# Performance work log

Hardware: AMD Instinct MI355X
Metric: run time of the kernel (lower is better)

The kernel has to match this reference:

```python
import jax, jax.numpy as jnp
import numpy as np

B, I, O, DEG = 16384, 1024, 1024, 8

def setup_inputs() -> dict:
    key = jax.random.key(0)
    kx, kc = jax.random.split(key)
    x = jax.random.normal(kx, (B, I), dtype=jnp.float32)
    std = 1.0 / (I * (DEG + 1))
    cheby_coeffs = jax.random.normal(kc, (I, O, DEG + 1), dtype=jnp.float32) * std
    return {"x": x, "cheby_coeffs": cheby_coeffs}


def reference(x, cheby_coeffs):
    # Chebyshev basis: T_d(tanh(x)) = cos(d * acos(tanh(x)))
    deg = cheby_coeffs.shape[-1]
    arange = jnp.arange(deg, dtype=x.dtype)  # (D+1,)
    theta = jnp.arccos(jnp.tanh(x))          # (B, I)
    basis = jnp.cos(theta[:, :, None] * arange)  # (B, I, D+1)
    y = jnp.einsum('bid,iod->bo', basis, cheby_coeffs)
    return y
```

## Files before the change

kernel.cpp:

```cpp
#include <hip/hip_runtime.h>
#include <hip/hip_bf16.h>


#define WSCALE 4096.0f
#define INV_WSCALE (1.0f/4096.0f)

typedef _Float16 f16;
typedef __fp16   hf2  __attribute__((ext_vector_type(2)));
typedef _Float16 f16x8 __attribute__((ext_vector_type(8)));
typedef float    f32x4 __attribute__((ext_vector_type(4)));
typedef float    f32x16 __attribute__((ext_vector_type(16)));

union F16x8u { hf2 h2[4]; f16x8 v8; };

__global__ __launch_bounds__(256) void wt_transform(const float* __restrict__ cc,
                                                    f16* __restrict__ wt) {
  int t    = blockIdx.x * 256 + threadIdx.x;
  int j4   = t & 127;
  int grp  = t >> 7;
  int ncol = grp & 7;
  int rest = grp >> 3;
  int ic   = rest & 31;
  int d    = rest >> 5;
  int u    = j4 >> 5;
  int h    = (j4 >> 4) & 1;
  int r    = j4 & 15;
  int rk   = (r >> 1) & 3;
  size_t base = (size_t)(d * 32 + ic) * 32768 + (size_t)ncol * 4096 + (size_t)j4 * 32;
#pragma unroll
  for (int v = 0; v < 4; ++v) {
    int tt = v ^ rk;
    int q  = tt & 1, kl = tt >> 1;
    int o  = ncol * 128 + u * 32 + q * 16 + r;
    int ib = ic * 32 + h * 16 + kl * 8;
    f16x8 val;
#pragma unroll
    for (int e = 0; e < 8; ++e)
      val[e] = (f16)(cc[((size_t)(ib + e) * 1024 + o) * 9 + d] * WSCALE);
    *(f16x8*)(wt + base + v * 8) = val;
  }
}

__global__ __launch_bounds__(256) void t2_transform(const float* __restrict__ x,
                                                    f16* __restrict__ t2) {
  size_t gid = (size_t)blockIdx.x * 256 + threadIdx.x;
  const float* p = x + gid * 8;
  f32x4 a = *(const f32x4*)p;
  f32x4 b = *(const f32x4*)(p + 4);
  float tf[8];
#pragma unroll
  for (int e = 0; e < 8; ++e) {
    float xx = (e < 4) ? a[e] : b[e - 4];
    tf[e] = 1.f - 2.f * __builtin_amdgcn_rcpf(__expf(2.f * xx) + 1.f);
  }
  F16x8u u;
#pragma unroll
  for (int q = 0; q < 4; ++q)
    u.h2[q] = __builtin_amdgcn_cvt_pkrtz(tf[2 * q], tf[2 * q + 1]);
  f16x8 v = u.v8 + u.v8;
  *(f16x8*)(t2 + gid * 8) = v;
}

template <int PRET>
__global__ __launch_bounds__(512, 2) void cheby_gemm(const float* __restrict__ x,
                                                     const f16* __restrict__ t2g,
                                                     const f16* __restrict__ wt,
                                                     float* __restrict__ out) {
  __shared__ f16 bbuf[18][4096];

  const int tid  = threadIdx.x;
  const int wid  = tid >> 6;
  const int lane = tid & 63;
  const int lr   = lane & 31;
  const int lh   = lane >> 5;
  const int wm   = wid >> 1;
  const int wn   = wid & 1;
  const int mrow = blockIdx.x >> 3;
  const int ncol = blockIdx.x & 7;
  const int m0   = mrow * 256 + wm * 64;
  const int n0   = ncol * 128 + wn * 64;
  const int rbase = wn * 2048 + ((lane & 15) * 4 + ((lane >> 4) ^ ((lane >> 1) & 3))) * 8;

  auto stage = [&](int cn, int dn, int buf) {
    const f16* src = wt + (size_t)(dn * 32 + cn) * 32768 + (size_t)ncol * 4096;
    __builtin_amdgcn_global_load_lds(
        (const __attribute__((address_space(1))) unsigned*)(src + tid * 8),
        (__attribute__((address_space(3))) unsigned*)(&bbuf[buf][wid * 512]),
        16, 0, 0);
  };
  auto stage9 = [&](int cn, int b0) {
#pragma unroll
    for (int d = 0; d < 9; ++d) stage(cn, d, b0 + d);
  };

  f32x16 acc[2][2];
#pragma unroll
  for (int a = 0; a < 2; ++a)
#pragma unroll
    for (int b = 0; b < 2; ++b)
#pragma unroll
      for (int j = 0; j < 16; ++j) acc[a][b][j] = 0.f;

  const f16x8 ones  = {(f16)1,(f16)1,(f16)1,(f16)1,(f16)1,(f16)1,(f16)1,(f16)1};
  const f16x8 half8 = {(f16)0.5f,(f16)0.5f,(f16)0.5f,(f16)0.5f,
                       (f16)0.5f,(f16)0.5f,(f16)0.5f,(f16)0.5f};
  f16x8 t2v[2][2], t2n[2][2];
  f32x4 xf[2][2][2];

  auto loadx = [&](int cn) {
    if constexpr (PRET) {
#pragma unroll
      for (int mb = 0; mb < 2; ++mb)
#pragma unroll
        for (int h = 0; h < 2; ++h)
          t2n[mb][h] = *(const f16x8*)(t2g + (size_t)(m0 + mb * 32 + lr) * 1024
                                           + cn * 32 + h * 16 + lh * 8);
    } else {
#pragma unroll
      for (int mb = 0; mb < 2; ++mb)
#pragma unroll
        for (int h = 0; h < 2; ++h) {
          const float* p = x + (size_t)(m0 + mb * 32 + lr) * 1024 + cn * 32 + h * 16 + lh * 8;
          xf[mb][h][0] = *(const f32x4*)p;
          xf[mb][h][1] = *(const f32x4*)(p + 4);
        }
    }
  };
  auto dotanh = [&]() {
    if constexpr (!PRET) {
#pragma unroll
      for (int mb = 0; mb < 2; ++mb)
#pragma unroll
        for (int h = 0; h < 2; ++h) {
          float tf[8];
#pragma unroll
          for (int e = 0; e < 8; ++e) {
            float xx = (e < 4) ? xf[mb][h][0][e] : xf[mb][h][1][e - 4];
            tf[e] = 1.f - 2.f * __builtin_amdgcn_rcpf(__expf(2.f * xx) + 1.f);
          }
          F16x8u u;
#pragma unroll
          for (int q = 0; q < 4; ++q)
            u.h2[q] = __builtin_amdgcn_cvt_pkrtz(tf[2 * q], tf[2 * q + 1]);
          t2n[mb][h] = u.v8 + u.v8;
        }
    }
  };

#define REC(NEW, S1, S2)                                                       \
  _Pragma("unroll") for (int mb = 0; mb < 2; ++mb)                             \
    _Pragma("unroll") for (int h = 0; h < 2; ++h)                              \
      NEW[mb][h] = __builtin_elementwise_fma(t2v[mb][h], S1[mb][h], -S2[mb][h]);

#define CLUSTER(AF, DIDX)                                                      \
  {                                                                            \
    const f16* bb = &bbuf[0][0] + sbase + (DIDX) * 4096 + rbase;               \
    f16x8 bf[2][2];                                                            \
    _Pragma("unroll") for (int nb = 0; nb < 2; ++nb)                           \
      _Pragma("unroll") for (int h = 0; h < 2; ++h)                            \
        bf[nb][h] = *(const f16x8*)&bb[nb * 1024 + h * 512];                   \
    _Pragma("unroll") for (int nb = 0; nb < 2; ++nb)                           \
      _Pragma("unroll") for (int mb = 0; mb < 2; ++mb) {                       \
        acc[mb][nb] = __builtin_amdgcn_mfma_f32_32x32x16_f16(AF[mb][0], bf[nb][0], \
                                                             acc[mb][nb], 0, 0, 0); \
        acc[mb][nb] = __builtin_amdgcn_mfma_f32_32x32x16_f16(AF[mb][1], bf[nb][1], \
                                                             acc[mb][nb], 0, 0, 0); \
      }                                                                        \
  }

  stage9(0, 0);
  loadx(0);
  dotanh();

  f16x8 onesA[2][2];
#pragma unroll
  for (int mb = 0; mb < 2; ++mb)
#pragma unroll
    for (int h = 0; h < 2; ++h) onesA[mb][h] = ones;

  for (int c = 0; c < 32; ++c) {
    const bool lastc = (c == 31);
    const int  sbase = (c & 1) * 9 * 4096;
    const int  nbase = (1 - (c & 1)) * 9;

    if constexpr (PRET) asm volatile("s_waitcnt vmcnt(4)" ::: "memory");
    else                asm volatile("s_waitcnt vmcnt(8)" ::: "memory");
    __builtin_amdgcn_s_barrier();

    f16x8 A1[2][2], A2[2][2], A3[2][2], A4[2][2], A5[2][2], A6[2][2], A7[2][2], A8[2][2];
#pragma unroll
    for (int mb = 0; mb < 2; ++mb)
#pragma unroll
      for (int h = 0; h < 2; ++h) {
        t2v[mb][h] = t2n[mb][h];
        A1[mb][h]  = t2v[mb][h] * half8;
      }

    if (!lastc) {
      stage9(c + 1, nbase);
      loadx(c + 1);
    }

    CLUSTER(onesA, 0)
    CLUSTER(A1, 1)
    REC(A2, A1, onesA)  CLUSTER(A2, 2)
    REC(A3, A2, A1)     CLUSTER(A3, 3)
    REC(A4, A3, A2)     CLUSTER(A4, 4)
    REC(A5, A4, A3)     CLUSTER(A5, 5)
    REC(A6, A5, A4)     CLUSTER(A6, 6)
    REC(A7, A6, A5)     CLUSTER(A7, 7)
    REC(A8, A7, A6)     CLUSTER(A8, 8)

    if (!lastc) dotanh();
  }
#undef REC
#undef CLUSTER

#pragma unroll
  for (int mb = 0; mb < 2; ++mb)
#pragma unroll
    for (int nb = 0; nb < 2; ++nb)
#pragma unroll
      for (int j = 0; j < 16; ++j) {
        int row = m0 + mb * 32 + 4 * lh + (j & 3) + 8 * (j >> 2);
        int col = n0 + nb * 32 + lr;
        out[(size_t)row * 1024 + col] = acc[mb][nb][j] * INV_WSCALE;
      }
}

extern "C" void kernel_launch(void* const* d_in, const int* in_sizes, int n_in,
                              void* d_out, int out_size, void* d_ws, size_t ws_size,
                              hipStream_t stream) {
  const float* x  = (const float*)d_in[0];
  const float* cc = (const float*)d_in[1];
  f16*   wt  = (f16*)d_ws;
  f16*   t2  = (f16*)((char*)d_ws + 18874368);
  float* out = (float*)d_out;

  hipLaunchKernelGGL(wt_transform, dim3(1152), dim3(256), 0, stream, cc, wt);
  if (ws_size >= 52428800) {
    hipLaunchKernelGGL(t2_transform, dim3(8192), dim3(256), 0, stream, x, t2);
    hipLaunchKernelGGL((cheby_gemm<1>), dim3(512), dim3(512), 0, stream, x, t2, wt, out);
  } else {
    hipLaunchKernelGGL((cheby_gemm<0>), dim3(512), dim3(512), 0, stream, x, t2, wt, out);
  }
}
```

Before: 328.6 us.

## Software-pipeline LDS fragment loads and per-degree staging in pretransformed GEMM

The pretransformed-input GEMM path is split into its own kernel. It interleaves the per-degree global-to-LDS staging for the next chunk with the compute of the current chunk, waiting on individual degree buffers instead of all nine at once. B fragments are double-buffered in registers so LDS reads overlap the MFMAs, and MFMA blocks raise wave priority with s_setprio. The last chunk is peeled out of the loop. The finer barriers add sync overhead in exchange for better overlap of memory and compute.

```diff
diff --git a/kernel.cpp b/kernel.cpp
--- a/kernel.cpp
+++ b/kernel.cpp
@@ -61,9 +61,7 @@
   *(f16x8*)(t2 + gid * 8) = v;
 }
 
-template <int PRET>
-__global__ __launch_bounds__(512, 2) void cheby_gemm(const float* __restrict__ x,
-                                                     const f16* __restrict__ t2g,
+__global__ __launch_bounds__(512, 2) void cheby_gemm(const f16* __restrict__ t2g,
                                                      const f16* __restrict__ wt,
                                                      float* __restrict__ out) {
   __shared__ f16 bbuf[18][4096];
@@ -88,6 +86,165 @@
         (__attribute__((address_space(3))) unsigned*)(&bbuf[buf][wid * 512]),
         16, 0, 0);
   };
+
+  f32x16 acc[2][2];
+#pragma unroll
+  for (int a = 0; a < 2; ++a)
+#pragma unroll
+    for (int b = 0; b < 2; ++b)
+#pragma unroll
+      for (int j = 0; j < 16; ++j) acc[a][b][j] = 0.f;
+
+  const f16x8 ones  = {(f16)1,(f16)1,(f16)1,(f16)1,(f16)1,(f16)1,(f16)1,(f16)1};
+  const f16x8 half8 = {(f16)0.5f,(f16)0.5f,(f16)0.5f,(f16)0.5f,
+                       (f16)0.5f,(f16)0.5f,(f16)0.5f,(f16)0.5f};
+  f16x8 t2v[2][2], t2n[2][2];
+
+  auto loadx = [&](int cn) {
+#pragma unroll
+    for (int mb = 0; mb < 2; ++mb)
+#pragma unroll
+      for (int h = 0; h < 2; ++h)
+        t2n[mb][h] = *(const f16x8*)(t2g + (size_t)(m0 + mb * 32 + lr) * 1024
+                                         + cn * 32 + h * 16 + lh * 8);
+  };
+
+#define REC(NEW, S1, S2)                                                       \
+  _Pragma("unroll") for (int mb = 0; mb < 2; ++mb)                             \
+    _Pragma("unroll") for (int h = 0; h < 2; ++h)                              \
+      NEW[mb][h] = __builtin_elementwise_fma(t2v[mb][h], S1[mb][h], -S2[mb][h]);
+
+#define LOADB(BD, SB, DIDX)                                                    \
+  {                                                                            \
+    const f16* bb = &bbuf[0][0] + (SB) + (DIDX) * 4096 + rbase;                \
+    BD[0][0] = *(const f16x8*)&bb[0];    BD[0][1] = *(const f16x8*)&bb[512];   \
+    BD[1][0] = *(const f16x8*)&bb[1024]; BD[1][1] = *(const f16x8*)&bb[1536];  \
+  }
+
+#define MFMA8(AF, BD)                                                          \
+  {                                                                            \
+    __builtin_amdgcn_s_setprio(1);                                             \
+    _Pragma("unroll") for (int nb = 0; nb < 2; ++nb)                           \
+      _Pragma("unroll") for (int mb = 0; mb < 2; ++mb) {                       \
+        acc[mb][nb] = __builtin_amdgcn_mfma_f32_32x32x16_f16(AF[mb][0], BD[nb][0], \
+                                                             acc[mb][nb], 0, 0, 0); \
+        acc[mb][nb] = __builtin_amdgcn_mfma_f32_32x32x16_f16(AF[mb][1], BD[nb][1], \
+                                                             acc[mb][nb], 0, 0, 0); \
+      }                                                                        \
+    __builtin_amdgcn_s_setprio(0);                                             \
+  }
+
+#define VMB(N)                                                                 \
+  asm volatile("s_waitcnt vmcnt(" #N ")" ::: "memory");                        \
+  __builtin_amdgcn_s_barrier();
+
+#pragma unroll
+  for (int d = 0; d < 9; ++d) stage(0, d, d);
+  loadx(0);
+
+  f16x8 onesA[2][2];
+#pragma unroll
+  for (int mb = 0; mb < 2; ++mb)
+#pragma unroll
+    for (int h = 0; h < 2; ++h) onesA[mb][h] = ones;
+
+  f16x8 bfA[2][2], bfB[2][2];
+  f16x8 A1[2][2], A2[2][2], A3[2][2], A4[2][2], A5[2][2], A6[2][2], A7[2][2], A8[2][2];
+
+  for (int c = 0; c < 31; ++c) {
+    const int sbase = (c & 1) * 36864;
+    const int nbase = (1 - (c & 1)) * 9;
+
+    VMB(7)
+    LOADB(bfA, sbase, 0)
+#pragma unroll
+    for (int mb = 0; mb < 2; ++mb)
+#pragma unroll
+      for (int h = 0; h < 2; ++h) {
+        t2v[mb][h] = t2n[mb][h];
+        A1[mb][h]  = t2v[mb][h] * half8;
+      }
+    stage(c + 1, 0, nbase + 0);
+    loadx(c + 1);
+    LOADB(bfB, sbase, 1)
+    MFMA8(onesA, bfA)
+
+    VMB(11) stage(c + 1, 1, nbase + 1); LOADB(bfA, sbase, 2) REC(A2, A1, onesA) MFMA8(A1, bfB)
+    VMB(11) stage(c + 1, 2, nbase + 2); LOADB(bfB, sbase, 3) REC(A3, A2, A1)    MFMA8(A2, bfA)
+    VMB(11) stage(c + 1, 3, nbase + 3); LOADB(bfA, sbase, 4) REC(A4, A3, A2)    MFMA8(A3, bfB)
+    VMB(11) stage(c + 1, 4, nbase + 4); LOADB(bfB, sbase, 5) REC(A5, A4, A3)    MFMA8(A4, bfA)
+    VMB(11) stage(c + 1, 5, nbase + 5); LOADB(bfA, sbase, 6) REC(A6, A5, A4)    MFMA8(A5, bfB)
+    VMB(11) stage(c + 1, 6, nbase + 6); LOADB(bfB, sbase, 7) REC(A7, A6, A5)    MFMA8(A6, bfA)
+    VMB(11) stage(c + 1, 7, nbase + 7); LOADB(bfA, sbase, 8) REC(A8, A7, A6)    MFMA8(A7, bfB)
+
+    stage(c + 1, 8, nbase + 8);
+    MFMA8(A8, bfA)
+  }
+
+  {
+    const int sbase = 36864;
+    asm volatile("s_waitcnt vmcnt(0)" ::: "memory");
+    __builtin_amdgcn_s_barrier();
+    LOADB(bfA, sbase, 0)
+#pragma unroll
+    for (int mb = 0; mb < 2; ++mb)
+#pragma unroll
+      for (int h = 0; h < 2; ++h) {
+        t2v[mb][h] = t2n[mb][h];
+        A1[mb][h]  = t2v[mb][h] * half8;
+      }
+    LOADB(bfB, sbase, 1)
+    MFMA8(onesA, bfA)
+    LOADB(bfA, sbase, 2) REC(A2, A1, onesA) MFMA8(A1, bfB)
+    LOADB(bfB, sbase, 3) REC(A3, A2, A1)    MFMA8(A2, bfA)
+    LOADB(bfA, sbase, 4) REC(A4, A3, A2)    MFMA8(A3, bfB)
+    LOADB(bfB, sbase, 5) REC(A5, A4, A3)    MFMA8(A4, bfA)
+    LOADB(bfA, sbase, 6) REC(A6, A5, A4)    MFMA8(A5, bfB)
+    LOADB(bfB, sbase, 7) REC(A7, A6, A5)    MFMA8(A6, bfA)
+    LOADB(bfA, sbase, 8) REC(A8, A7, A6)    MFMA8(A7, bfB)
+    MFMA8(A8, bfA)
+  }
+#undef REC
+#undef LOADB
+#undef MFMA8
+#undef VMB
+
+#pragma unroll
+  for (int mb = 0; mb < 2; ++mb)
+#pragma unroll
+    for (int nb = 0; nb < 2; ++nb)
+#pragma unroll
+      for (int j = 0; j < 16; ++j) {
+        int row = m0 + mb * 32 + 4 * lh + (j & 3) + 8 * (j >> 2);
+        int col = n0 + nb * 32 + lr;
+        out[(size_t)row * 1024 + col] = acc[mb][nb][j] * INV_WSCALE;
+      }
+}
+
+__global__ __launch_bounds__(512, 2) void cheby_gemm_fb(const float* __restrict__ x,
+                                                        const f16* __restrict__ wt,
+                                                        float* __restrict__ out) {
+  __shared__ f16 bbuf[18][4096];
+  const int tid  = threadIdx.x;
+  const int wid  = tid >> 6;
+  const int lane = tid & 63;
+  const int lr   = lane & 31;
+  const int lh   = lane >> 5;
+  const int wm   = wid >> 1;
+  const int wn   = wid & 1;
+  const int mrow = blockIdx.x >> 3;
+  const int ncol = blockIdx.x & 7;
+  const int m0   = mrow * 256 + wm * 64;
+  const int n0   = ncol * 128 + wn * 64;
+  const int rbase = wn * 2048 + ((lane & 15) * 4 + ((lane >> 4) ^ ((lane >> 1) & 3))) * 8;
+
+  auto stage = [&](int cn, int dn, int buf) {
+    const f16* src = wt + (size_t)(dn * 32 + cn) * 32768 + (size_t)ncol * 4096;
+    __builtin_amdgcn_global_load_lds(
+        (const __attribute__((address_space(1))) unsigned*)(src + tid * 8),
+        (__attribute__((address_space(3))) unsigned*)(&bbuf[buf][wid * 512]),
+        16, 0, 0);
+  };
   auto stage9 = [&](int cn, int b0) {
 #pragma unroll
     for (int d = 0; d < 9; ++d) stage(cn, d, b0 + d);
@@ -108,50 +265,38 @@
   f32x4 xf[2][2][2];
 
   auto loadx = [&](int cn) {
-    if constexpr (PRET) {
-#pragma unroll
-      for (int mb = 0; mb < 2; ++mb)
-#pragma unroll
-        for (int h = 0; h < 2; ++h)
-          t2n[mb][h] = *(const f16x8*)(t2g + (size_t)(m0 + mb * 32 + lr) * 1024
-                                           + cn * 32 + h * 16 + lh * 8);
-    } else {
-#pragma unroll
-      for (int mb = 0; mb < 2; ++mb)
-#pragma unroll
-        for (int h = 0; h < 2; ++h) {
-          const float* p = x + (size_t)(m0 + mb * 32 + lr) * 1024 + cn * 32 + h * 16 + lh * 8;
-          xf[mb][h][0] = *(const f32x4*)p;
-          xf[mb][h][1] = *(const f32x4*)(p + 4);
+#pragma unroll
+    for (int mb = 0; mb < 2; ++mb)
+#pragma unroll
+      for (int h = 0; h < 2; ++h) {
+        const float* p = x + (size_t)(m0 + mb * 32 + lr) * 1024 + cn * 32 + h * 16 + lh * 8;
+        xf[mb][h][0] = *(const f32x4*)p;
+        xf[mb][h][1] = *(const f32x4*)(p + 4);
+      }
+  };
+  auto dotanh = [&]() {
+#pragma unroll
+    for (int mb = 0; mb < 2; ++mb)
+#pragma unroll
+      for (int h = 0; h < 2; ++h) {
+        float tf[8];
+#pragma unroll
+        for (int e = 0; e < 8; ++e) {
+          float xx = (e < 4) ? xf[mb][h][0][e] : xf[mb][h][1][e - 4];
+          tf[e] = 1.f - 2.f * __builtin_amdgcn_rcpf(__expf(2.f * xx) + 1.f);
         }
-    }
-  };
-  auto dotanh = [&]() {
-    if constexpr (!PRET) {
-#pragma unroll
-      for (int mb = 0; mb < 2; ++mb)
-#pragma unroll
-        for (int h = 0; h < 2; ++h) {
-          float tf[8];
-#pragma unroll
-          for (int e = 0; e < 8; ++e) {
-            float xx = (e < 4) ? xf[mb][h][0][e] : xf[mb][h][1][e - 4];
-            tf[e] = 1.f - 2.f * __builtin_amdgcn_rcpf(__expf(2.f * xx) + 1.f);
-          }
-          F16x8u u;
-#pragma unroll
-          for (int q = 0; q < 4; ++q)
-            u.h2[q] = __builtin_amdgcn_cvt_pkrtz(tf[2 * q], tf[2 * q + 1]);
-          t2n[mb][h] = u.v8 + u.v8;
-        }
-    }
+        F16x8u u;
+#pragma unroll
+        for (int q = 0; q < 4; ++q)
+          u.h2[q] = __builtin_amdgcn_cvt_pkrtz(tf[2 * q], tf[2 * q + 1]);
+        t2n[mb][h] = u.v8 + u.v8;
+      }
   };
 
 #define REC(NEW, S1, S2)                                                       \
   _Pragma("unroll") for (int mb = 0; mb < 2; ++mb)                             \
     _Pragma("unroll") for (int h = 0; h < 2; ++h)                              \
       NEW[mb][h] = __builtin_elementwise_fma(t2v[mb][h], S1[mb][h], -S2[mb][h]);
-
 #define CLUSTER(AF, DIDX)                                                      \
   {                                                                            \
     const f16* bb = &bbuf[0][0] + sbase + (DIDX) * 4096 + rbase;               \
@@ -180,11 +325,10 @@
 
   for (int c = 0; c < 32; ++c) {
     const bool lastc = (c == 31);
-    const int  sbase = (c & 1) * 9 * 4096;
+    const int  sbase = (c & 1) * 36864;
     const int  nbase = (1 - (c & 1)) * 9;
 
-    if constexpr (PRET) asm volatile("s_waitcnt vmcnt(4)" ::: "memory");
-    else                asm volatile("s_waitcnt vmcnt(8)" ::: "memory");
+    asm volatile("s_waitcnt vmcnt(8)" ::: "memory");
     __builtin_amdgcn_s_barrier();
 
     f16x8 A1[2][2], A2[2][2], A3[2][2], A4[2][2], A5[2][2], A6[2][2], A7[2][2], A8[2][2];
@@ -195,11 +339,7 @@
         t2v[mb][h] = t2n[mb][h];
         A1[mb][h]  = t2v[mb][h] * half8;
       }
-
-    if (!lastc) {
-      stage9(c + 1, nbase);
-      loadx(c + 1);
-    }
+    if (!lastc) { stage9(c + 1, nbase); loadx(c + 1); }
 
     CLUSTER(onesA, 0)
     CLUSTER(A1, 1)
@@ -210,7 +350,6 @@
     REC(A6, A5, A4)     CLUSTER(A6, 6)
     REC(A7, A6, A5)     CLUSTER(A7, 7)
     REC(A8, A7, A6)     CLUSTER(A8, 8)
-
     if (!lastc) dotanh();
   }
 #undef REC
@@ -240,8 +379,8 @@
   hipLaunchKernelGGL(wt_transform, dim3(1152), dim3(256), 0, stream, cc, wt);
   if (ws_size >= 52428800) {
     hipLaunchKernelGGL(t2_transform, dim3(8192), dim3(256), 0, stream, x, t2);
-    hipLaunchKernelGGL((cheby_gemm<1>), dim3(512), dim3(512), 0, stream, x, t2, wt, out);
+    hipLaunchKernelGGL(cheby_gemm, dim3(512), dim3(512), 0, stream, t2, wt, out);
   } else {
-    hipLaunchKernelGGL((cheby_gemm<0>), dim3(512), dim3(512), 0, stream, x, t2, wt, out);
-  }
-}
+    hipLaunchKernelGGL(cheby_gemm_fb, dim3(512), dim3(512), 0, stream, x, wt, out);
+  }
+}
```

After: 333.3 us. No clear change (+1.4%).
